# Performance work log

Measured on AMD Instinct MI355X. Metric: run time of the kernel, lower is better.

Reference implementation:

```python
import jax, jax.numpy as jnp
import numpy as np

N_NODES = 50000
N_EDGES = 800000
F_IN = 128          # num_node_features == conv_size
L = 4               # num_conv_layers
LIN = 256
OUT = 10
N_GRAPHS = 64


def setup_inputs() -> dict:
    key = jax.random.key(0)
    ks = jax.random.split(key, 8)
    x = jax.random.normal(ks[0], (N_NODES, F_IN), dtype=jnp.float32)
    edge_index = jax.random.randint(ks[1], (2, N_EDGES), 0, N_NODES, dtype=jnp.int64)
    batch = jnp.sort(jax.random.randint(ks[2], (N_NODES,), 0, N_GRAPHS, dtype=jnp.int64))
    pos = jax.random.normal(ks[3], (N_NODES, 3), dtype=jnp.float32)
    # learned params: 4 GCN layers (all [F_IN,F_IN] since in==out==128), cat-JK head
    Ws = jax.random.normal(ks[4], (L, F_IN, F_IN), dtype=jnp.float32) * 0.05
    bs = jnp.zeros((L, F_IN), dtype=jnp.float32)
    Wlin = jax.random.normal(ks[5], (L * F_IN, LIN), dtype=jnp.float32) * 0.05
    blin = jnp.zeros((LIN,), dtype=jnp.float32)
    Wout = jax.random.normal(ks[6], (LIN, OUT), dtype=jnp.float32) * 0.05
    bout = jnp.zeros((OUT,), dtype=jnp.float32)
    return {"x": x, "edge_index": edge_index, "batch": batch, "pos": pos,
            "Ws": Ws, "bs": bs, "Wlin": Wlin, "blin": blin,
            "Wout": Wout, "bout": bout}


def reference(x, edge_index, batch, pos, Ws, bs, Wlin, blin, Wout, bout):
    N = x.shape[0]
    # GCN normalization with added self-loops (PyG gcn_norm, edge_weight=1)
    loop = jnp.arange(N, dtype=edge_index.dtype)
    src = jnp.concatenate([edge_index[0], loop])
    dst = jnp.concatenate([edge_index[1], loop])
    deg = jax.ops.segment_sum(jnp.ones_like(dst, dtype=x.dtype), dst, num_segments=N)
    dinv = jax.lax.rsqrt(deg)  # deg >= 1 due to self-loops
    norm = (dinv[src] * dinv[dst])[:, None]  # [E+N, 1]

    h = x
    xs = []
    for l in range(L):
        t = h @ Ws[l]                                    # [N, F]
        agg = jax.ops.segment_sum(t[src] * norm, dst, num_segments=N)
        h = jax.nn.relu(agg + bs[l])                     # dropout is identity in eval
        xs.append(h)
    hcat = jnp.concatenate(xs, axis=-1)                  # JK 'cat' -> [N, L*F]
    g = jax.ops.segment_max(hcat, batch, num_segments=N_GRAPHS)  # global_max_pool
    return jax.nn.relu(g @ Wlin + blin) @ Wout + bout    # [N_GRAPHS, OUT]
```

## Files before the change

### kernel.cpp

```cpp
#include <hip/hip_runtime.h>
#include <stdint.h>

#define NN    50000
#define NE    800000
#define FD    128
#define NLAY  4
#define NLIN  256
#define NOUTF 10
#define NGR   64
#define NBKT  196
#define MAXB  8192

typedef _Float16 half8  __attribute__((ext_vector_type(8)));
typedef _Float16 half4  __attribute__((ext_vector_type(4)));
typedef _Float16 half2t __attribute__((ext_vector_type(2)));
typedef float    f32x4  __attribute__((ext_vector_type(4)));

__device__ __forceinline__ int ld_idx(const void* p, int flag, long i){
    return flag ? (int)((const long long*)p)[i] : ((const int*)p)[i];
}

__global__ __launch_bounds__(256) void pre_k(const unsigned* __restrict__ eidx_u,
                                             const float* __restrict__ Ws,
                                             _Float16* __restrict__ WT,
                                             int* __restrict__ zbase, int zn, int zb,
                                             int* __restrict__ sent,
                                             int* __restrict__ flag){
    __shared__ int any;
    const int b = blockIdx.x, tid = threadIdx.x;
    if (b < 256){
        int idx = b*256 + tid;
        int l = idx >> 14;
        int r = idx & 16383;
        int c = r >> 7, k = r & 127;
        WT[idx] = (_Float16)Ws[(l<<14) + (k<<7) + c];
    } else if (b < 256 + zb){
        int i = (b-256)*256 + tid;
        if (i < zn) zbase[i] = 0;
    } else if (b == 256 + zb){
        if (tid < FD/2) sent[tid] = 0;
    } else {
        if (tid == 0) any = 0;
        __syncthreads();
        if (eidx_u[2*tid + 1] != 0u) atomicOr(&any, 1);
        __syncthreads();
        if (tid == 0) *flag = (any == 0) ? 1 : 0;
    }
}

__global__ __launch_bounds__(1024) void binB_k(const void* __restrict__ eidx,
                                               const int* __restrict__ flag,
                                               int* __restrict__ bktCur,
                                               unsigned* __restrict__ binned){
    __shared__ int hist[NBKT];
    __shared__ int resv[NBKT];
    __shared__ int cur[NBKT];
    const int tid = threadIdx.x;
    const int f = *flag;
    if (tid < NBKT){ hist[tid] = 0; cur[tid] = 0; }
    __syncthreads();

    int bkt[4]; unsigned pk[4];
    #pragma unroll
    for (int u = 0; u < 4; ++u){
        long e = (long)blockIdx.x*4096 + u*1024 + tid;
        if (e < NE){
            int s = ld_idx(eidx, f, e);
            int d = ld_idx(eidx, f, (long)NE + e);
            bkt[u] = d >> 8;
            pk[u]  = ((unsigned)(d & 255) << 16) | (unsigned)s;
            atomicAdd(&hist[bkt[u]], 1);
        } else bkt[u] = -1;
    }
    __syncthreads();
    if (tid < NBKT && hist[tid] > 0)
        resv[tid] = atomicAdd(&bktCur[tid], hist[tid]);
    __syncthreads();
    #pragma unroll
    for (int u = 0; u < 4; ++u){
        if (bkt[u] >= 0){
            int p = resv[bkt[u]] + atomicAdd(&cur[bkt[u]], 1);
            if (p < MAXB) binned[(long)bkt[u]*MAXB + p] = pk[u];
        }
    }
}

__global__ __launch_bounds__(256) void passC_k(const int* __restrict__ bktCur,
                                               const unsigned* __restrict__ binned,
                                               int* __restrict__ rp, int* __restrict__ re,
                                               float* __restrict__ dinv,
                                               unsigned short* __restrict__ cn,
                                               const void* __restrict__ batv,
                                               const int* __restrict__ flag,
                                               int* __restrict__ gstart){
    __shared__ unsigned staged[MAXB];
    __shared__ int cnt[256];
    __shared__ int sc[256];
    __shared__ int cur[256];
    const int tid = threadIdx.x;
    if (blockIdx.x >= NBKT){
        int i = (blockIdx.x - NBKT)*256 + tid;
        if (i >= NN) return;
        int f = *flag;
        int b = ld_idx(batv, f, i);
        if (i == 0){
            for (int g = 0; g <= b; ++g) gstart[g] = 0;
        } else {
            int p = ld_idx(batv, f, i-1);
            for (int g = p+1; g <= b; ++g) gstart[g] = i;
        }
        if (i == NN-1){
            for (int g = b+1; g <= NGR; ++g) gstart[g] = NN;
        }
        return;
    }
    const int b = blockIdx.x;
    int n = bktCur[b]; if (n > MAXB) n = MAXB;
    const long base = (long)b*MAXB;

    cnt[tid] = 0;
    __syncthreads();
    for (int i = tid; i < n; i += 256){
        unsigned rec = binned[base + i];
        staged[i] = rec;
        atomicAdd(&cnt[rec >> 16], 1);
    }
    __syncthreads();
    int c  = cnt[tid];
    int pc = (c + 15) & ~15;
    sc[tid] = pc;
    __syncthreads();
    for (int off = 1; off < 256; off <<= 1){
        int t = (tid >= off) ? sc[tid - off] : 0;
        __syncthreads();
        if (tid >= off) sc[tid] += t;
        __syncthreads();
    }
    int lo = sc[tid] - pc;
    int v = b*256 + tid;
    if (v < NN){
        rp[v]   = (int)base + lo;
        re[v]   = (int)base + lo + pc;
        dinv[v] = rsqrtf((float)(c + 1));
    }
    cur[tid] = lo;
    __syncthreads();
    for (int i = tid; i < n; i += 256){
        unsigned rec = staged[i];
        int j = rec >> 16;
        int p = atomicAdd(&cur[j], 1);
        cn[base + p] = (unsigned short)(rec & 0xFFFFu);
    }
    __syncthreads();
    for (int i = c; i < pc; ++i)
        cn[base + lo + i] = (unsigned short)NN;
}

template<bool F32IN>
__global__ __launch_bounds__(256) void gemm_k(const void* __restrict__ Av,
                                              const _Float16* __restrict__ WT,
                                              const float* __restrict__ dinv,
                                              _Float16* __restrict__ T){
    const int tid  = threadIdx.x;
    const int lane = tid & 63;
    const int wid  = tid >> 6;
    const int wr   = (wid >> 1) * 32;
    const int wc   = (wid & 1) * 64;
    const long r0  = (long)blockIdx.x * 64 + wr;
    const int lr   = lane & 15;
    const int lk   = (lane >> 4) * 8;

    half8 wf[4][4];
    #pragma unroll
    for (int n = 0; n < 4; ++n)
        #pragma unroll
        for (int kk = 0; kk < 4; ++kk)
            wf[n][kk] = *reinterpret_cast<const half8*>(WT + (wc + n*16 + lr)*FD + kk*32 + lk);

    f32x4 acc[2][4];
    #pragma unroll
    for (int m = 0; m < 2; ++m)
        #pragma unroll
        for (int n = 0; n < 4; ++n)
            acc[m][n] = (f32x4){0.f,0.f,0.f,0.f};

    #pragma unroll
    for (int kk = 0; kk < 4; ++kk){
        half8 af[2];
        #pragma unroll
        for (int m = 0; m < 2; ++m){
            long row = r0 + m*16 + lr;
            if (row < NN){
                if constexpr (F32IN){
                    const float* A = (const float*)Av;
                    float4 u0 = *reinterpret_cast<const float4*>(A + row*FD + kk*32 + lk);
                    float4 u1 = *reinterpret_cast<const float4*>(A + row*FD + kk*32 + lk + 4);
                    half8 a;
                    a[0]=(_Float16)u0.x; a[1]=(_Float16)u0.y; a[2]=(_Float16)u0.z; a[3]=(_Float16)u0.w;
                    a[4]=(_Float16)u1.x; a[5]=(_Float16)u1.y; a[6]=(_Float16)u1.z; a[7]=(_Float16)u1.w;
                    af[m] = a;
                } else {
                    const _Float16* A = (const _Float16*)Av;
                    af[m] = *reinterpret_cast<const half8*>(A + row*FD + kk*32 + lk);
                }
            } else af[m] = (half8)(_Float16)0;
        }
        #pragma unroll
        for (int m = 0; m < 2; ++m)
            #pragma unroll
            for (int n = 0; n < 4; ++n)
                acc[m][n] = __builtin_amdgcn_mfma_f32_16x16x32_f16(wf[n][kk], af[m], acc[m][n], 0, 0, 0);
    }

    #pragma unroll
    for (int m = 0; m < 2; ++m){
        long row = r0 + m*16 + lr;
        if (row >= NN) continue;
        float di = dinv[row];
        #pragma unroll
        for (int n = 0; n < 4; ++n){
            half4 o;
            o[0] = (_Float16)(acc[m][n][0] * di);
            o[1] = (_Float16)(acc[m][n][1] * di);
            o[2] = (_Float16)(acc[m][n][2] * di);
            o[3] = (_Float16)(acc[m][n][3] * di);
            *reinterpret_cast<half4*>(T + row*FD + wc + n*16 + (lane>>4)*4) = o;
        }
    }
}

__global__ __launch_bounds__(256) void agg_k(const _Float16* __restrict__ t,
                                             const int* __restrict__ rp,
                                             const int* __restrict__ re,
                                             const unsigned short* __restrict__ cn,
                                             const float* __restrict__ dinv,
                                             const float* __restrict__ bias,
                                             _Float16* __restrict__ h){
    const int lane = threadIdx.x & 63;
    const int wid  = threadIdx.x >> 6;
    const int r    = lane & 15;
    const int qb   = lane & 48;
    const int v    = blockIdx.x*16 + wid*4 + (lane >> 4);
    const half8* t8 = reinterpret_cast<const half8*>(t);

    float acc[8];
    #pragma unroll
    for (int i = 0; i < 8; ++i) acc[i] = 0.f;

    half8 sv = t8[(size_t)v*16 + r];

    const int e0 = rp[v], e1 = re[v];
    for (int base = e0; base < e1; base += 16){
        int ce = (int)cn[base + r];
        #pragma unroll
        for (int j = 0; j < 16; ++j){
            int s = __shfl(ce, qb + j);
            half8 g = t8[(size_t)s*16 + r];
            #pragma unroll
            for (int i = 0; i < 8; ++i) acc[i] += (float)g[i];
        }
    }

    float di = dinv[v];
    float4 b0 = reinterpret_cast<const float4*>(bias)[2*r];
    float4 b1 = reinterpret_cast<const float4*>(bias)[2*r+1];
    float bb[8] = {b0.x,b0.y,b0.z,b0.w,b1.x,b1.y,b1.z,b1.w};
    half8 o;
    #pragma unroll
    for (int i = 0; i < 8; ++i)
        o[i] = (_Float16)fmaxf(fmaf(acc[i] + (float)sv[i], di, bb[i]), 0.f);
    reinterpret_cast<half8*>(h)[(size_t)v*16 + r] = o;
}

__global__ __launch_bounds__(256) void pool_k(const _Float16* __restrict__ h,
                                              const int* __restrict__ gstart,
                                              unsigned* __restrict__ gbuf, int l){
    __shared__ float red[4][FD];
    int g = blockIdx.x, part = blockIdx.y;
    int tid = threadIdx.x, lane = tid & 63, w = tid >> 6;
    int s0 = gstart[g], s1 = gstart[g+1];
    int len = s1 - s0;
    int chunk = (len + 7) >> 3;
    int a = s0 + part*chunk;
    int b = min(a + chunk, s1);
    int sub = (b - a + 3) >> 2;
    int aa = a + w*sub;
    int bb = min(aa + sub, b);
    const half2t* h2 = reinterpret_cast<const half2t*>(h);
    float m0 = 0.f, m1 = 0.f;
    for (int i = aa; i < bb; ++i){
        half2t x = h2[(long)i*64 + lane];
        m0 = fmaxf(m0, (float)x[0]);
        m1 = fmaxf(m1, (float)x[1]);
    }
    red[w][2*lane]   = m0;
    red[w][2*lane+1] = m1;
    __syncthreads();
    if (w == 0){
        float r0 = fmaxf(fmaxf(red[0][2*lane],   red[1][2*lane]),
                         fmaxf(red[2][2*lane],   red[3][2*lane]));
        float r1 = fmaxf(fmaxf(red[0][2*lane+1], red[1][2*lane+1]),
                         fmaxf(red[2][2*lane+1], red[3][2*lane+1]));
        atomicMax(&gbuf[g*(NLAY*FD) + l*FD + 2*lane    ], __float_as_uint(r0));
        atomicMax(&gbuf[g*(NLAY*FD) + l*FD + 2*lane + 1], __float_as_uint(r1));
    }
}

__global__ __launch_bounds__(1024) void head_k(const unsigned* __restrict__ gbuf,
                                               const float* __restrict__ Wlin,
                                               const float* __restrict__ blin,
                                               const float* __restrict__ Wout,
                                               const float* __restrict__ bout,
                                               float* __restrict__ out){
    __shared__ float gs[NLAY*FD];
    __shared__ float ps[4][NLIN];
    __shared__ float us[NLIN];
    int g = blockIdx.x, tid = threadIdx.x;
    if (tid < NLAY*FD) gs[tid] = __uint_as_float(gbuf[g*(NLAY*FD) + tid]);
    __syncthreads();
    int c = tid & 255;
    int q = tid >> 8;
    float a = 0.f;
    #pragma unroll 8
    for (int k = q*128; k < q*128 + 128; ++k)
        a = fmaf(gs[k], Wlin[k*NLIN + c], a);
    ps[q][c] = a;
    __syncthreads();
    if (tid < NLIN){
        float u = ps[0][tid] + ps[1][tid] + ps[2][tid] + ps[3][tid] + blin[tid];
        us[tid] = fmaxf(u, 0.f);
    }
    __syncthreads();
    if (tid < NOUTF){
        float o = bout[tid];
        #pragma unroll 8
        for (int k = 0; k < NLIN; ++k) o = fmaf(us[k], Wout[k*NOUTF + tid], o);
        out[g*NOUTF + tid] = o;
    }
}

extern "C" void kernel_launch(void* const* d_in, const int* in_sizes, int n_in,
                              void* d_out, int out_size, void* d_ws, size_t ws_size,
                              hipStream_t stream){
    const float* x    = (const float*)d_in[0];
    const void*  eidx = d_in[1];
    const void*  batv = d_in[2];
    const float* Wsp  = (const float*)d_in[4];
    const float* bsp  = (const float*)d_in[5];
    const float* Wlin = (const float*)d_in[6];
    const float* blin = (const float*)d_in[7];
    const float* Wout = (const float*)d_in[8];
    const float* bout = (const float*)d_in[9];
    float* out = (float*)d_out;

    uintptr_t cur = (uintptr_t)d_ws;
    auto alloc = [&](size_t bytes)->void*{
        cur = (cur + 255) & ~(uintptr_t)255;
        void* p = (void*)cur;
        cur += bytes;
        return p;
    };
    _Float16* t    = (_Float16*)alloc((size_t)(NN+1)*FD*2);
    _Float16* h    = (_Float16*)alloc((size_t)NN*FD*2);
    _Float16* WT   = (_Float16*)alloc((size_t)NLAY*FD*FD*2);
    unsigned* binned = (unsigned*)alloc((size_t)NBKT*MAXB*4);
    unsigned short* cn = (unsigned short*)alloc((size_t)NBKT*MAXB*2);
    int*   rp    = (int*)  alloc((size_t)NN*4);
    int*   re    = (int*)  alloc((size_t)NN*4);
    float* dinv  = (float*)alloc((size_t)NN*4);
    int*   gst   = (int*)  alloc((NGR+1)*4);
    int*   flag  = (int*)  alloc(4);
    int*      bktCur = (int*)     alloc((size_t)NBKT*4);
    unsigned* gbuf   = (unsigned*)alloc((size_t)NGR*NLAY*FD*4);
    int zero_n = (int)((cur - (uintptr_t)bktCur + 3) / 4);
    int zb = (zero_n + 255) / 256;

    pre_k  <<<256 + zb + 2, 256, 0, stream>>>((const unsigned*)eidx, Wsp, WT,
                                              bktCur, zero_n, zb,
                                              (int*)(t + (size_t)NN*FD), flag);
    binB_k <<<NBKT, 1024, 0, stream>>>(eidx, flag, bktCur, binned);
    passC_k<<<NBKT + (NN+255)/256, 256, 0, stream>>>(bktCur, binned, rp, re, dinv, cn,
                                                     batv, flag, gst);

    for (int l = 0; l < NLAY; ++l){
        const void* hin = (l == 0) ? (const void*)x : (const void*)h;
        if (l == 0)
            gemm_k<true ><<<(NN+63)/64, 256, 0, stream>>>(hin, WT + (size_t)l*FD*FD, dinv, t);
        else
            gemm_k<false><<<(NN+63)/64, 256, 0, stream>>>(hin, WT + (size_t)l*FD*FD, dinv, t);
        agg_k<<<NN/16, 256, 0, stream>>>(t, rp, re, cn, dinv, bsp + (size_t)l*FD, h);
        pool_k<<<dim3(NGR, 8), 256, 0, stream>>>(h, gst, gbuf, l);
    }
    head_k<<<NGR, 1024, 0, stream>>>(gbuf, Wlin, blin, Wout, bout, out);
}
```

Before: 281.4 us.

## Fold per-layer max-pool into next layer's GEMM launch as extra blocks

The global max-pool for layer l-1 now runs as extra blocks appended to layer l's GEMM grid. This removes three separate pool kernel launches and lets pooling overlap with the GEMM on otherwise idle CUs. The final layer still uses a standalone pool kernel. It adds branching inside the GEMM kernel and may raise shared-memory use for all blocks, which could lower GEMM occupancy.

After: 262.1 us. -6.9%, faster.

```diff
diff --git a/kernel.cpp b/kernel.cpp
--- a/kernel.cpp
+++ b/kernel.cpp
@@ -10,6 +10,8 @@
 #define NGR   64
 #define NBKT  196
 #define MAXB  8192
+#define GEMMB 782
+#define POOLB 512
 
 typedef _Float16 half8  __attribute__((ext_vector_type(8)));
 typedef _Float16 half4  __attribute__((ext_vector_type(4)));
@@ -80,7 +82,7 @@
     for (int u = 0; u < 4; ++u){
         if (bkt[u] >= 0){
             int p = resv[bkt[u]] + atomicAdd(&cur[bkt[u]], 1);
-            if (p < MAXB) binned[(long)bkt[u]*MAXB + p] = pk[u];
+            if ((unsigned)p < MAXB) binned[(long)bkt[u]*MAXB + p] = pk[u];
         }
     }
 }
@@ -156,12 +158,49 @@
         cn[base + lo + i] = (unsigned short)NN;
 }
 
-template<bool F32IN>
+template<bool F32IN, bool POOL>
 __global__ __launch_bounds__(256) void gemm_k(const void* __restrict__ Av,
                                               const _Float16* __restrict__ WT,
                                               const float* __restrict__ dinv,
-                                              _Float16* __restrict__ T){
+                                              _Float16* __restrict__ T,
+                                              const _Float16* __restrict__ h,
+                                              const int* __restrict__ gstart,
+                                              unsigned* __restrict__ gbuf, int lpool){
     const int tid  = threadIdx.x;
+    if (POOL && blockIdx.x >= GEMMB){
+        __shared__ float red[4][FD];
+        int pid = blockIdx.x - GEMMB;
+        int g = pid >> 3, part = pid & 7;
+        int lane = tid & 63, w = tid >> 6;
+        int s0 = gstart[g], s1 = gstart[g+1];
+        int len = s1 - s0;
+        int chunk = (len + 7) >> 3;
+        int a = s0 + part*chunk;
+        int b = min(a + chunk, s1);
+        int sub = (b - a + 3) >> 2;
+        int aa = a + w*sub;
+        int bb = min(aa + sub, b);
+        const half2t* h2 = reinterpret_cast<const half2t*>(h);
+        float m0 = 0.f, m1 = 0.f;
+        for (int i = aa; i < bb; ++i){
+            half2t x = h2[(long)i*64 + lane];
+            m0 = fmaxf(m0, (float)x[0]);
+            m1 = fmaxf(m1, (float)x[1]);
+        }
+        red[w][2*lane]   = m0;
+        red[w][2*lane+1] = m1;
+        __syncthreads();
+        if (w == 0){
+            float r0 = fmaxf(fmaxf(red[0][2*lane],   red[1][2*lane]),
+                             fmaxf(red[2][2*lane],   red[3][2*lane]));
+            float r1 = fmaxf(fmaxf(red[0][2*lane+1], red[1][2*lane+1]),
+                             fmaxf(red[2][2*lane+1], red[3][2*lane+1]));
+            atomicMax(&gbuf[g*(NLAY*FD) + lpool*FD + 2*lane    ], __float_as_uint(r0));
+            atomicMax(&gbuf[g*(NLAY*FD) + lpool*FD + 2*lane + 1], __float_as_uint(r1));
+        }
+        return;
+    }
+
     const int lane = tid & 63;
     const int wid  = tid >> 6;
     const int wr   = (wid >> 1) * 32;
@@ -385,11 +424,13 @@
     for (int l = 0; l < NLAY; ++l){
         const void* hin = (l == 0) ? (const void*)x : (const void*)h;
         if (l == 0)
-            gemm_k<true ><<<(NN+63)/64, 256, 0, stream>>>(hin, WT + (size_t)l*FD*FD, dinv, t);
+            gemm_k<true ,false><<<GEMMB, 256, 0, stream>>>(hin, WT, dinv, t,
+                                                           h, gst, gbuf, 0);
         else
-            gemm_k<false><<<(NN+63)/64, 256, 0, stream>>>(hin, WT + (size_t)l*FD*FD, dinv, t);
+            gemm_k<false,true ><<<GEMMB + POOLB, 256, 0, stream>>>(hin, WT + (size_t)l*FD*FD,
+                                                                   dinv, t, h, gst, gbuf, l-1);
         agg_k<<<NN/16, 256, 0, stream>>>(t, rp, re, cn, dinv, bsp + (size_t)l*FD, h);
-        pool_k<<<dim3(NGR, 8), 256, 0, stream>>>(h, gst, gbuf, l);
-    }
+    }
+    pool_k<<<dim3(NGR, 8), 256, 0, stream>>>(h, gst, gbuf, NLAY-1);
     head_k<<<NGR, 1024, 0, stream>>>(gbuf, Wlin, blin, Wout, bout, out);
 }
```
